# Kernel optimization log

Hardware: AMD Instinct MI355X
Metric: run time of the kernel (lower is better)

Reference implementation:

```python
import jax, jax.numpy as jnp
import numpy as np

DIM = 512
HEADS = 16
WH, WW = 8, 8
B, NW = 8, 64
HD = DIM // HEADS            # 32, head dim
DR = HD // 2                 # 16, rotary dim per spatial axis
LN100 = float(np.log(100.0))


def _axial_freqs():
    # rotary-embedding-torch get_axial_freqs: per-axis freqs (interleaved repeat)
    inv = 1.0 / (10000.0 ** (np.arange(0, DR, 2, dtype=np.float32) / DR))  # (DR/2,)
    fh = np.repeat(np.arange(WH, dtype=np.float32)[:, None] * inv[None, :], 2, axis=-1)  # (WH, DR)
    fw = np.repeat(np.arange(WW, dtype=np.float32)[:, None] * inv[None, :], 2, axis=-1)  # (WW, DR)
    fh = np.broadcast_to(fh[:, None, :], (WH, WW, DR))
    fw = np.broadcast_to(fw[None, :, :], (WH, WW, DR))
    return jnp.asarray(np.concatenate([fh, fw], axis=-1))  # (WH, WW, HD)


def _rotate_half(t):
    # interleaved-pair rotation: (x0,x1) -> (-x1,x0)
    x = t.reshape(t.shape[:-1] + (t.shape[-1] // 2, 2))
    return jnp.stack([-x[..., 1], x[..., 0]], axis=-1).reshape(t.shape)


def _apply_rope(t, freqs):
    return t * jnp.cos(freqs) + _rotate_half(t) * jnp.sin(freqs)


def setup_inputs() -> dict:
    key = jax.random.key(0)
    k0, k1, k2 = jax.random.split(key, 3)
    x = jax.random.normal(k0, (B, NW, WH * WW, DIM), jnp.float32)
    qkv_weight = jax.random.normal(k1, (3 * DIM, DIM), jnp.float32) * 0.02
    q_bias = jnp.zeros((DIM,), jnp.float32)
    v_bias = jnp.zeros((DIM,), jnp.float32)
    logit_scale = jnp.full((HEADS, 1, 1, 1), float(np.log(10.0)), jnp.float32)
    proj_weight = jax.random.normal(k2, (DIM, DIM), jnp.float32) * 0.02
    proj_bias = jnp.zeros((DIM,), jnp.float32)
    return {"x": x, "qkv_weight": qkv_weight, "q_bias": q_bias, "v_bias": v_bias,
            "logit_scale": logit_scale, "proj_weight": proj_weight, "proj_bias": proj_bias}


def reference(x, qkv_weight, q_bias, v_bias, logit_scale, proj_weight, proj_bias):
    Bx, Nw, N, C = x.shape
    qkv_b = jnp.concatenate([q_bias, jnp.zeros_like(v_bias), v_bias])
    qkv = x @ qkv_weight.T + qkv_b                                   # (B, Nw, N, 3C)
    qkv = qkv.reshape(Bx, Nw, N, 3, HEADS, HD).transpose(3, 0, 4, 1, 2, 5)  # (3, B, H, Nw, N, hd)
    q, k, v = qkv[0], qkv[1], qkv[2]
    # cosine attention: L2-normalize q, k
    q = q / jnp.maximum(jnp.linalg.norm(q, axis=-1, keepdims=True), 1e-12)
    k = k / jnp.maximum(jnp.linalg.norm(k, axis=-1, keepdims=True), 1e-12)
    q = jnp.exp(jnp.clip(logit_scale, LN100, None)) * q             # per-head scale, clamp min=ln(100)
    # axial RoPE over the (Wh, Ww) window grid
    freqs = _axial_freqs()                                           # (WH, WW, HD)
    q = _apply_rope(q.reshape(Bx, HEADS, Nw, WH, WW, HD), freqs).reshape(Bx, HEADS, Nw, N, HD)
    k = _apply_rope(k.reshape(Bx, HEADS, Nw, WH, WW, HD), freqs).reshape(Bx, HEADS, Nw, N, HD)
    # block-diagonal (per-window) attention; flex_attention default scale 1/sqrt(hd)
    scores = jnp.einsum('bhwqd,bhwkd->bhwqk', q, k) * (1.0 / np.sqrt(HD))
    attn = jax.nn.softmax(scores, axis=-1)
    out = jnp.einsum('bhwqk,bhwkd->bhwqd', attn, v)                  # (B, H, Nw, N, hd)
    out = out.transpose(0, 2, 3, 1, 4).reshape(Bx, Nw, N, C)
    return out @ proj_weight.T + proj_bias
```

## Files before the change

kernel.cpp:

```cpp
#include <hip/hip_runtime.h>
#include <stdint.h>

#define DIMC   512
#define NHEADS 16
#define HDIM   32
#define NWIN   64
#define NTOK   64
#define NBATCH 8
#define MROWS  (NBATCH * NWIN * NTOK)

typedef unsigned short ushort_t;
typedef __attribute__((ext_vector_type(8))) short short8v;
typedef __attribute__((ext_vector_type(4))) float f32x4;

__device__ inline ushort_t f2bf(float f) {
    unsigned u = __float_as_uint(f);
    u += 0x7FFFu + ((u >> 16) & 1u);
    return (ushort_t)(u >> 16);
}
__device__ inline unsigned packbf2(float a, float b) {
    return ((unsigned)f2bf(a)) | (((unsigned)f2bf(b)) << 16);
}
__device__ inline void unpack8(uint4 u, float* f) {
    const unsigned a[4] = {u.x, u.y, u.z, u.w};
    #pragma unroll
    for (int j = 0; j < 4; ++j) {
        f[2*j+0] = __uint_as_float((a[j] & 0xFFFFu) << 16);
        f[2*j+1] = __uint_as_float(a[j] & 0xFFFF0000u);
    }
}

#define G2L16(gp, lp) __builtin_amdgcn_global_load_lds( \
    (const __attribute__((address_space(1))) unsigned int*)(gp), \
    (__attribute__((address_space(3))) unsigned int*)(lp), 16, 0, 0)

__global__ __launch_bounds__(256) void cvt_f32_bf16(
    const float* __restrict__ in, ushort_t* __restrict__ out, int n4)
{
    int i = blockIdx.x * 256 + threadIdx.x;
    if (i < n4) {
        float4 v = reinterpret_cast<const float4*>(in)[i];
        ushort4 o;
        o.x = f2bf(v.x); o.y = f2bf(v.y); o.z = f2bf(v.z); o.w = f2bf(v.w);
        reinterpret_cast<ushort4*>(out)[i] = o;
    }
}

__global__ void build_qkv_bias(const float* __restrict__ qb,
                               const float* __restrict__ vb,
                               float* __restrict__ bias)
{
    int i = blockIdx.x * 256 + threadIdx.x;
    if (i < 3 * DIMC) {
        float v = 0.f;
        if (i < DIMC) v = qb[i];
        else if (i >= 2 * DIMC) v = vb[i - 2 * DIMC];
        bias[i] = v;
    }
}

template<bool OUT_BF16>
__global__ __launch_bounds__(256) void gemm_bt_128(
    const ushort_t* __restrict__ A, const ushort_t* __restrict__ B,
    const float* __restrict__ bias, void* __restrict__ C,
    int M, int N, int K)
{
    __shared__ ushort_t lsA[128 * 32];
    __shared__ ushort_t lsB[128 * 32];

    const int tid = threadIdx.x;
    const int l   = tid & 63;
    const int wv  = tid >> 6;
    const int wr  = wv >> 1;
    const int wc  = wv & 1;
    const size_t mBase = (size_t)blockIdx.y * 128;
    const size_t nBase = (size_t)blockIdx.x * 128;

    f32x4 acc[4][4] = {};

    const ushort_t* gA0 = A + (mBase + (size_t)(wv * 16 + (l >> 2))) * (size_t)K + (l & 3) * 8;
    const ushort_t* gB0 = B + (nBase + (size_t)(wv * 16 + (l >> 2))) * (size_t)K + (l & 3) * 8;
    ushort_t* lA0 = &lsA[(wv * 16) * 32];
    ushort_t* lB0 = &lsB[(wv * 16) * 32];
    const size_t rowStep = (size_t)64 * (size_t)K;

    for (int k0 = 0; k0 < K; k0 += 32) {
        G2L16(gA0 + k0,           lA0);
        G2L16(gA0 + k0 + rowStep, lA0 + 64 * 32);
        G2L16(gB0 + k0,           lB0);
        G2L16(gB0 + k0 + rowStep, lB0 + 64 * 32);
        __syncthreads();

        short8v aF[4], bF[4];
        #pragma unroll
        for (int m = 0; m < 4; ++m)
            aF[m] = *reinterpret_cast<const short8v*>(
                &lsA[(wr * 64 + m * 16 + (l & 15)) * 32 + (l >> 4) * 8]);
        #pragma unroll
        for (int n = 0; n < 4; ++n)
            bF[n] = *reinterpret_cast<const short8v*>(
                &lsB[(wc * 64 + n * 16 + (l & 15)) * 32 + (l >> 4) * 8]);

        #pragma unroll
        for (int m = 0; m < 4; ++m)
            #pragma unroll
            for (int n = 0; n < 4; ++n)
                acc[m][n] = __builtin_amdgcn_mfma_f32_16x16x32_bf16(
                    aF[m], bF[n], acc[m][n], 0, 0, 0);
        __syncthreads();
    }

    const int c0 = l & 15;
    const int r0 = (l >> 4) * 4;
    #pragma unroll
    for (int m = 0; m < 4; ++m) {
        #pragma unroll
        for (int n = 0; n < 4; ++n) {
            const size_t gn = nBase + (size_t)(wc * 64 + n * 16 + c0);
            const float bv = bias[gn];
            #pragma unroll
            for (int i = 0; i < 4; ++i) {
                const size_t gm = mBase + (size_t)(wr * 64 + m * 16 + r0 + i);
                const float val = acc[m][n][i] + bv;
                if (OUT_BF16) ((ushort_t*)C)[gm * (size_t)N + gn] = f2bf(val);
                else          ((float*)C)  [gm * (size_t)N + gn] = val;
            }
        }
    }
}

__global__ __launch_bounds__(64, 3) void win_attn_mfma(
    const ushort_t* __restrict__ qkv,
    const float* __restrict__ logit_scale,
    ushort_t* __restrict__ attn_out)
{
    __shared__ __align__(16) ushort_t lsP[64 * 64];
    __shared__ __align__(16) ushort_t lsV[2 * 64 * 16];
    __shared__ float2 csT[8][8];

    const int l = threadIdx.x;
    const int c = l & 15;
    const int g = l >> 4;
    const int blk = blockIdx.x;
    const int w = blk & 63;
    const int h = (blk >> 6) & 15;
    const int b = blk >> 10;
    const size_t R = ((size_t)(b * 64 + w)) * 64;
    const ushort_t* qrow = qkv + R * 1536 + h * 32;

    {
        const ushort_t* vbase = qrow + 1024;
        #pragma unroll
        for (int half = 0; half < 2; ++half)
            #pragma unroll
            for (int kg = 0; kg < 2; ++kg) {
                const ushort_t* gsrc = vbase + (size_t)(kg * 32 + (l >> 1)) * 1536
                                       + half * 16 + (l & 1) * 8;
                G2L16(gsrc, &lsV[half * 1024 + kg * 512]);
            }
    }

    {
        const int pos = l >> 3, f = l & 7;
        const float inv = __expf(-(float)f * 1.1512925464970230f);
        const float ang = (float)pos * inv;
        csT[pos][f] = make_float2(__cosf(ang), __sinf(ang));
    }

    const float sc = __expf(fmaxf(logit_scale[h], 4.6051701859880914f))
                     * 0.17677669529663687f;

    short8v Qf[4], Kf[4];
    #pragma unroll
    for (int mi = 0; mi < 4; ++mi) {
        const int tok = mi * 16 + c;
        const ushort_t* qp = qrow + (size_t)tok * 1536 + g * 8;
        uint4 uq = *reinterpret_cast<const uint4*>(qp);
        uint4 uk = *reinterpret_cast<const uint4*>(qp + 512);
        float qv[8], kv[8];
        unpack8(uq, qv); unpack8(uk, kv);

        float sq = 0.f, sk = 0.f;
        #pragma unroll
        for (int d = 0; d < 8; ++d) { sq += qv[d] * qv[d]; sk += kv[d] * kv[d]; }
        sq += __shfl_xor(sq, 16); sq += __shfl_xor(sq, 32);
        sk += __shfl_xor(sk, 16); sk += __shfl_xor(sk, 32);
        const float qs = sc * rsqrtf(fmaxf(sq, 1e-24f));
        const float ks =      rsqrtf(fmaxf(sk, 1e-24f));

        const int wh = tok >> 3, ww = tok & 7;
        const int axpos = (g >= 2) ? ww : wh;
        union { short8v v; unsigned u[4]; } pq, pk2;
        #pragma unroll
        for (int pp = 0; pp < 4; ++pp) {
            const float2 cs = csT[axpos][(g & 1) * 4 + pp];
            float a0 = qv[2*pp] * qs, a1 = qv[2*pp+1] * qs;
            const float q0 = a0 * cs.x - a1 * cs.y;
            const float q1 = a1 * cs.x + a0 * cs.y;
            a0 = kv[2*pp] * ks; a1 = kv[2*pp+1] * ks;
            const float k0 = a0 * cs.x - a1 * cs.y;
            const float k1 = a1 * cs.x + a0 * cs.y;
            pq.u[pp]  = packbf2(q0, q1);
            pk2.u[pp] = packbf2(k0, k1);
        }
        Qf[mi] = pq.v; Kf[mi] = pk2.v;
    }

    f32x4 S[4][4];
    #pragma unroll
    for (int ki = 0; ki < 4; ++ki)
        #pragma unroll
        for (int qi = 0; qi < 4; ++qi)
            S[ki][qi] = __builtin_amdgcn_mfma_f32_16x16x32_bf16(
                Kf[ki], Qf[qi], (f32x4){0.f, 0.f, 0.f, 0.f}, 0, 0, 0);

    float isum[4];
    #pragma unroll
    for (int qi = 0; qi < 4; ++qi) {
        float m = -1e30f;
        #pragma unroll
        for (int ki = 0; ki < 4; ++ki)
            #pragma unroll
            for (int i = 0; i < 4; ++i) m = fmaxf(m, S[ki][qi][i]);
        m = fmaxf(m, __shfl_xor(m, 16));
        m = fmaxf(m, __shfl_xor(m, 32));
        float sum = 0.f;
        #pragma unroll
        for (int ki = 0; ki < 4; ++ki)
            #pragma unroll
            for (int i = 0; i < 4; ++i) {
                const float p = __expf(S[ki][qi][i] - m);
                S[ki][qi][i] = p; sum += p;
            }
        sum += __shfl_xor(sum, 16); sum += __shfl_xor(sum, 32);
        isum[qi] = 1.0f / sum;
    }

    #pragma unroll
    for (int qi = 0; qi < 4; ++qi) {
        const int q = qi * 16 + c;
        #pragma unroll
        for (int ki = 0; ki < 4; ++ki) {
            const int s2 = 2 * ki + (g >> 1);
            const int byteoff = q * 128 + ((s2 ^ (q & 7)) * 16) + (g & 1) * 8;
            uint2 pk2;
            pk2.x = packbf2(S[ki][qi][0], S[ki][qi][1]);
            pk2.y = packbf2(S[ki][qi][2], S[ki][qi][3]);
            *reinterpret_cast<uint2*>(reinterpret_cast<char*>(lsP) + byteoff) = pk2;
        }
    }

    asm volatile("s_waitcnt vmcnt(0)" ::: "memory");
    short8v Vf[2][2];
    #pragma unroll
    for (int half = 0; half < 2; ++half)
        #pragma unroll
        for (int ki = 0; ki < 2; ++ki) {
            union { short8v v; ushort_t e[8]; } t;
            #pragma unroll
            for (int j = 0; j < 8; ++j)
                t.e[j] = lsV[half * 1024 + (ki * 32 + g * 8 + j) * 16 + c];
            Vf[half][ki] = t.v;
        }

    short8v Pf[4][2];
    #pragma unroll
    for (int ni = 0; ni < 4; ++ni) {
        const int q = ni * 16 + c;
        #pragma unroll
        for (int ki = 0; ki < 2; ++ki) {
            const int s2 = ki * 4 + g;
            Pf[ni][ki] = *reinterpret_cast<const short8v*>(
                reinterpret_cast<const char*>(lsP) + q * 128 + ((s2 ^ (q & 7)) * 16));
        }
    }

    f32x4 O[2][4];
    #pragma unroll
    for (int mi = 0; mi < 2; ++mi)
        #pragma unroll
        for (int ni = 0; ni < 4; ++ni) {
            f32x4 a = __builtin_amdgcn_mfma_f32_16x16x32_bf16(
                Vf[mi][0], Pf[ni][0], (f32x4){0.f, 0.f, 0.f, 0.f}, 0, 0, 0);
            O[mi][ni] = __builtin_amdgcn_mfma_f32_16x16x32_bf16(
                Vf[mi][1], Pf[ni][1], a, 0, 0, 0);
        }

    #pragma unroll
    for (int ni = 0; ni < 4; ++ni) {
        const int q = ni * 16 + c;
        const float is = isum[ni];
        #pragma unroll
        for (int mi = 0; mi < 2; ++mi) {
            const int s = 2 * mi + (g >> 1);
            const int byteoff = q * 64 + ((s ^ (q & 3)) * 16) + (g & 1) * 8;
            uint2 pk2;
            pk2.x = packbf2(O[mi][ni][0] * is, O[mi][ni][1] * is);
            pk2.y = packbf2(O[mi][ni][2] * is, O[mi][ni][3] * is);
            *reinterpret_cast<uint2*>(reinterpret_cast<char*>(lsP) + byteoff) = pk2;
        }
    }

    const int qr0 = l >> 2, p = l & 3;
    ushort_t* obase = attn_out + R * 512 + h * 32;
    #pragma unroll
    for (int r = 0; r < 4; ++r) {
        const int q = qr0 + r * 16;
        uint4 row = *reinterpret_cast<const uint4*>(
            reinterpret_cast<const char*>(lsP) + q * 64 + ((p ^ (q & 3)) * 16));
        *reinterpret_cast<uint4*>(
            reinterpret_cast<char*>(obase + (size_t)q * 512) + p * 16) = row;
    }
}

extern "C" void kernel_launch(void* const* d_in, const int* in_sizes, int n_in,
                              void* d_out, int out_size, void* d_ws, size_t ws_size,
                              hipStream_t stream)
{
    (void)in_sizes; (void)n_in; (void)out_size; (void)ws_size;
    const float* x     = (const float*)d_in[0];
    const float* wqkv  = (const float*)d_in[1];
    const float* qb    = (const float*)d_in[2];
    const float* vb    = (const float*)d_in[3];
    const float* ls    = (const float*)d_in[4];
    const float* wproj = (const float*)d_in[5];
    const float* pb    = (const float*)d_in[6];
    float* out = (float*)d_out;

    char* ws = (char*)d_ws;
    ushort_t* xb      = (ushort_t*)(ws);
    ushort_t* wqkvb   = (ushort_t*)(ws + 33554432);
    ushort_t* wprojb  = (ushort_t*)(ws + 35127296);
    ushort_t* qkvb    = (ushort_t*)(ws + 35651584);
    ushort_t* attnb   = (ushort_t*)(ws + 136314880);
    float*    qkvbias = (float*)   (ws + 169869312);

    cvt_f32_bf16<<<16384, 256, 0, stream>>>(x,     xb,     16777216 / 4);
    cvt_f32_bf16<<<768,   256, 0, stream>>>(wqkv,  wqkvb,  786432   / 4);
    cvt_f32_bf16<<<256,   256, 0, stream>>>(wproj, wprojb, 262144   / 4);
    build_qkv_bias<<<6, 256, 0, stream>>>(qb, vb, qkvbias);

    gemm_bt_128<true><<<dim3(12, 256), 256, 0, stream>>>(
        xb, wqkvb, qkvbias, qkvb, MROWS, 3 * DIMC, DIMC);

    win_attn_mfma<<<NBATCH * NHEADS * NWIN, 64, 0, stream>>>(qkvb, ls, attnb);

    gemm_bt_128<false><<<dim3(4, 256), 256, 0, stream>>>(
        attnb, wprojb, pb, out, MROWS, DIMC, DIMC);
}
```

Measured before the change: 276.7 us.

## Double GEMM K-tile to 64 with XOR-swizzled LDS layout

The bf16 GEMM kernels now stage a 64-wide K slice per iteration instead of 32, halving the number of barrier pairs per output tile and issuing twice as many MFMAs between syncs. The LDS layout is XOR-swizzled by row so that 16-byte fragment reads from the 128-byte rows avoid bank conflicts. Shared memory per block doubles to 32 KB, which may reduce how many blocks fit per CU.

New measurement: 271.2 us. 2.0% less time.

```diff
diff --git a/kernel.cpp b/kernel.cpp
--- a/kernel.cpp
+++ b/kernel.cpp
@@ -60,13 +60,13 @@
 }
 
 template<bool OUT_BF16>
-__global__ __launch_bounds__(256) void gemm_bt_128(
+__global__ __launch_bounds__(256) void gemm_bt_128x64(
     const ushort_t* __restrict__ A, const ushort_t* __restrict__ B,
     const float* __restrict__ bias, void* __restrict__ C,
     int M, int N, int K)
 {
-    __shared__ ushort_t lsA[128 * 32];
-    __shared__ ushort_t lsB[128 * 32];
+    __shared__ ushort_t lsA[128 * 64];
+    __shared__ ushort_t lsB[128 * 64];
 
     const int tid = threadIdx.x;
     const int l   = tid & 63;
@@ -78,35 +78,45 @@
 
     f32x4 acc[4][4] = {};
 
-    const ushort_t* gA0 = A + (mBase + (size_t)(wv * 16 + (l >> 2))) * (size_t)K + (l & 3) * 8;
-    const ushort_t* gB0 = B + (nBase + (size_t)(wv * 16 + (l >> 2))) * (size_t)K + (l & 3) * 8;
-    ushort_t* lA0 = &lsA[(wv * 16) * 32];
-    ushort_t* lB0 = &lsB[(wv * 16) * 32];
-    const size_t rowStep = (size_t)64 * (size_t)K;
-
-    for (int k0 = 0; k0 < K; k0 += 32) {
-        G2L16(gA0 + k0,           lA0);
-        G2L16(gA0 + k0 + rowStep, lA0 + 64 * 32);
-        G2L16(gB0 + k0,           lB0);
-        G2L16(gB0 + k0 + rowStep, lB0 + 64 * 32);
+    const int rl    = l >> 3;
+    const int chunk = (l & 7) ^ rl;
+    const ushort_t* gA0 = A + (mBase + (size_t)(wv * 32 + rl)) * (size_t)K + chunk * 8;
+    const ushort_t* gB0 = B + (nBase + (size_t)(wv * 32 + rl)) * (size_t)K + chunk * 8;
+    ushort_t* lA0 = &lsA[(wv * 32) * 64];
+    ushort_t* lB0 = &lsB[(wv * 32) * 64];
+
+    for (int k0 = 0; k0 < K; k0 += 64) {
+        #pragma unroll
+        for (int j = 0; j < 4; ++j) {
+            G2L16(gA0 + (size_t)(j * 8) * (size_t)K + k0, lA0 + j * 8 * 64);
+            G2L16(gB0 + (size_t)(j * 8) * (size_t)K + k0, lB0 + j * 8 * 64);
+        }
         __syncthreads();
 
-        short8v aF[4], bF[4];
-        #pragma unroll
-        for (int m = 0; m < 4; ++m)
-            aF[m] = *reinterpret_cast<const short8v*>(
-                &lsA[(wr * 64 + m * 16 + (l & 15)) * 32 + (l >> 4) * 8]);
-        #pragma unroll
-        for (int n = 0; n < 4; ++n)
-            bF[n] = *reinterpret_cast<const short8v*>(
-                &lsB[(wc * 64 + n * 16 + (l & 15)) * 32 + (l >> 4) * 8]);
-
-        #pragma unroll
-        for (int m = 0; m < 4; ++m)
-            #pragma unroll
-            for (int n = 0; n < 4; ++n)
-                acc[m][n] = __builtin_amdgcn_mfma_f32_16x16x32_bf16(
-                    aF[m], bF[n], acc[m][n], 0, 0, 0);
+        #pragma unroll
+        for (int kk = 0; kk < 2; ++kk) {
+            short8v aF[4], bF[4];
+            #pragma unroll
+            for (int m = 0; m < 4; ++m) {
+                const int row = wr * 64 + m * 16 + (l & 15);
+                const int ps  = (kk * 4 + (l >> 4)) ^ (row & 7);
+                aF[m] = *reinterpret_cast<const short8v*>(
+                    reinterpret_cast<const char*>(lsA) + row * 128 + ps * 16);
+            }
+            #pragma unroll
+            for (int n = 0; n < 4; ++n) {
+                const int row = wc * 64 + n * 16 + (l & 15);
+                const int ps  = (kk * 4 + (l >> 4)) ^ (row & 7);
+                bF[n] = *reinterpret_cast<const short8v*>(
+                    reinterpret_cast<const char*>(lsB) + row * 128 + ps * 16);
+            }
+            #pragma unroll
+            for (int m = 0; m < 4; ++m)
+                #pragma unroll
+                for (int n = 0; n < 4; ++n)
+                    acc[m][n] = __builtin_amdgcn_mfma_f32_16x16x32_bf16(
+                        aF[m], bF[n], acc[m][n], 0, 0, 0);
+        }
         __syncthreads();
     }
 
@@ -340,11 +350,11 @@
     cvt_f32_bf16<<<256,   256, 0, stream>>>(wproj, wprojb, 262144   / 4);
     build_qkv_bias<<<6, 256, 0, stream>>>(qb, vb, qkvbias);
 
-    gemm_bt_128<true><<<dim3(12, 256), 256, 0, stream>>>(
+    gemm_bt_128x64<true><<<dim3(12, 256), 256, 0, stream>>>(
         xb, wqkvb, qkvbias, qkvb, MROWS, 3 * DIMC, DIMC);
 
     win_attn_mfma<<<NBATCH * NHEADS * NWIN, 64, 0, stream>>>(qkvb, ls, attnb);
 
-    gemm_bt_128<false><<<dim3(4, 256), 256, 0, stream>>>(
+    gemm_bt_128x64<false><<<dim3(4, 256), 256, 0, stream>>>(
         attnb, wprojb, pb, out, MROWS, DIMC, DIMC);
 }
```

## Replace GEMM with 256x256 double-buffered, swizzled, phase-pipelined MFMA kernel

Applied to the files above, without the earlier changes.

Both projection GEMMs move from a 128x128 single-buffered tile kernel to a 512-thread 256x256 tile kernel with BK=64. It double-buffers LDS, uses XOR-swizzled LDS layouts, and splits each K step into four phases that interleave global-to-LDS staging with MFMA quadrants under explicit barriers and waitcnts. The block index is remapped across XCD-style groups, and MFMA sections raise wave priority. This aims to hide memory latency and increase reuse, at the cost of large LDS use (128KB per block), lower occupancy and fragile manual synchronisation. A __syncthreads is also added in the attention kernel before LDS reuse.

Measured after the change: 285.2 us. 1.03x slower.

```diff
diff --git a/kernel.cpp b/kernel.cpp
--- a/kernel.cpp
+++ b/kernel.cpp
@@ -59,68 +59,133 @@
     }
 }
 
+#define BARX() { asm volatile("" ::: "memory"); \
+                 __builtin_amdgcn_s_barrier();  \
+                 asm volatile("" ::: "memory"); }
+#define LGKM0() asm volatile("s_waitcnt lgkmcnt(0)" ::: "memory")
+#define VMW(n)  asm volatile("s_waitcnt vmcnt(" #n ")" ::: "memory")
+
+#define STAGE(ls, g, bufi, t, h)                                             \
+    {                                                                        \
+        const int _k0 = (t) << 6;                                            \
+        _Pragma("unroll")                                                    \
+        for (int _r = 0; _r < 2; ++_r)                                       \
+            G2L16(g + (size_t)((h) * 128 + _r * 64) * (size_t)K + _k0,       \
+                  &ls[bufi][((h) * 128 + _r * 64 + wv * 8) * 64]);           \
+    }
+
+#define DSA(dst, bufi, mh)                                                   \
+    _Pragma("unroll")                                                        \
+    for (int _m = 0; _m < 4; ++_m) {                                         \
+        _Pragma("unroll")                                                    \
+        for (int _k = 0; _k < 2; ++_k) {                                     \
+            const int _row = wr * 128 + ((mh) * 4 + _m) * 16 + (l & 15);     \
+            const int _ps  = (_k * 4 + (l >> 4)) ^ (_row & 7);               \
+            dst[_m * 2 + _k] = *reinterpret_cast<const short8v*>(            \
+                reinterpret_cast<const char*>(lsA[bufi]) + _row * 128 + _ps * 16); \
+        }                                                                    \
+    }
+
+#define DSB(dst, bufi, nh)                                                   \
+    _Pragma("unroll")                                                        \
+    for (int _n = 0; _n < 2; ++_n) {                                         \
+        _Pragma("unroll")                                                    \
+        for (int _k = 0; _k < 2; ++_k) {                                     \
+            const int _row = wc * 64 + ((nh) * 2 + _n) * 16 + (l & 15);      \
+            const int _ps  = (_k * 4 + (l >> 4)) ^ (_row & 7);               \
+            dst[_n * 2 + _k] = *reinterpret_cast<const short8v*>(            \
+                reinterpret_cast<const char*>(lsB[bufi]) + _row * 128 + _ps * 16); \
+        }                                                                    \
+    }
+
+#define MMQ(af, bf, mo, no)                                                  \
+    __builtin_amdgcn_s_setprio(1);                                           \
+    _Pragma("unroll")                                                        \
+    for (int _m = 0; _m < 4; ++_m) {                                         \
+        _Pragma("unroll")                                                    \
+        for (int _n = 0; _n < 2; ++_n) {                                     \
+            _Pragma("unroll")                                                \
+            for (int _k = 0; _k < 2; ++_k)                                   \
+                acc[(mo) + _m][(no) + _n] =                                  \
+                    __builtin_amdgcn_mfma_f32_16x16x32_bf16(                 \
+                        af[_m * 2 + _k], bf[_n * 2 + _k],                    \
+                        acc[(mo) + _m][(no) + _n], 0, 0, 0);                 \
+        }                                                                    \
+    }                                                                        \
+    __builtin_amdgcn_s_setprio(0);
+
 template<bool OUT_BF16>
-__global__ __launch_bounds__(256) void gemm_bt_128(
+__global__ __launch_bounds__(512, 2) void gemm_bt_8ph(
     const ushort_t* __restrict__ A, const ushort_t* __restrict__ B,
     const float* __restrict__ bias, void* __restrict__ C,
-    int M, int N, int K)
+    int N, int K, int nx)
 {
-    __shared__ ushort_t lsA[128 * 32];
-    __shared__ ushort_t lsB[128 * 32];
+    __shared__ ushort_t lsA[2][256 * 64];
+    __shared__ ushort_t lsB[2][256 * 64];
 
     const int tid = threadIdx.x;
     const int l   = tid & 63;
     const int wv  = tid >> 6;
-    const int wr  = wv >> 1;
-    const int wc  = wv & 1;
-    const size_t mBase = (size_t)blockIdx.y * 128;
-    const size_t nBase = (size_t)blockIdx.x * 128;
-
-    f32x4 acc[4][4] = {};
-
-    const ushort_t* gA0 = A + (mBase + (size_t)(wv * 16 + (l >> 2))) * (size_t)K + (l & 3) * 8;
-    const ushort_t* gB0 = B + (nBase + (size_t)(wv * 16 + (l >> 2))) * (size_t)K + (l & 3) * 8;
-    ushort_t* lA0 = &lsA[(wv * 16) * 32];
-    ushort_t* lB0 = &lsB[(wv * 16) * 32];
-    const size_t rowStep = (size_t)64 * (size_t)K;
-
-    for (int k0 = 0; k0 < K; k0 += 32) {
-        G2L16(gA0 + k0,           lA0);
-        G2L16(gA0 + k0 + rowStep, lA0 + 64 * 32);
-        G2L16(gB0 + k0,           lB0);
-        G2L16(gB0 + k0 + rowStep, lB0 + 64 * 32);
-        __syncthreads();
-
-        short8v aF[4], bF[4];
-        #pragma unroll
-        for (int m = 0; m < 4; ++m)
-            aF[m] = *reinterpret_cast<const short8v*>(
-                &lsA[(wr * 64 + m * 16 + (l & 15)) * 32 + (l >> 4) * 8]);
-        #pragma unroll
-        for (int n = 0; n < 4; ++n)
-            bF[n] = *reinterpret_cast<const short8v*>(
-                &lsB[(wc * 64 + n * 16 + (l & 15)) * 32 + (l >> 4) * 8]);
-
-        #pragma unroll
-        for (int m = 0; m < 4; ++m)
-            #pragma unroll
-            for (int n = 0; n < 4; ++n)
-                acc[m][n] = __builtin_amdgcn_mfma_f32_16x16x32_bf16(
-                    aF[m], bF[n], acc[m][n], 0, 0, 0);
-        __syncthreads();
+    const int wr  = wv >> 2;
+    const int wc  = wv & 3;
+
+    const int nwg = (int)gridDim.x;
+    const int bid = (int)blockIdx.x;
+    const int swz = (bid & 7) * (nwg >> 3) + (bid >> 3);
+    const size_t mBase = (size_t)(swz / nx) * 256;
+    const size_t nBase = (size_t)(swz % nx) * 256;
+
+    f32x4 acc[8][4] = {};
+
+    const int srow   = l >> 3;
+    const int schunk = (l & 7) ^ srow;
+    const ushort_t* gA = A + (mBase + (size_t)(wv * 8 + srow)) * (size_t)K + schunk * 8;
+    const ushort_t* gB = B + (nBase + (size_t)(wv * 8 + srow)) * (size_t)K + schunk * 8;
+
+    STAGE(lsA, gA, 0, 0, 0); STAGE(lsA, gA, 0, 0, 1);
+    STAGE(lsB, gB, 0, 0, 0); STAGE(lsB, gB, 0, 0, 1);
+    STAGE(lsB, gB, 1, 1, 0); STAGE(lsB, gB, 1, 1, 1);
+    VMW(4);
+    BARX();
+
+    short8v aF[8], bF[4], bF2[4];
+    const int nt = K >> 6;
+    for (int t = 0; t < nt; ++t) {
+        const int buf = t & 1, nbuf = buf ^ 1;
+        DSA(aF, buf, 0);
+        DSB(bF, buf, 0);
+        if (t + 1 < nt) STAGE(lsA, gA, nbuf, t + 1, 0);
+        BARX(); LGKM0();
+        MMQ(aF, bF, 0, 0);
+        BARX();
+        DSB(bF2, buf, 1);
+        if (t + 1 < nt) STAGE(lsA, gA, nbuf, t + 1, 1);
+        BARX(); LGKM0();
+        MMQ(aF, bF2, 0, 2);
+        BARX();
+        DSA(aF, buf, 1);
+        if (t + 2 < nt) STAGE(lsB, gB, buf, t + 2, 0);
+        BARX(); LGKM0();
+        MMQ(aF, bF, 4, 0);
+        BARX();
+        if (t + 2 < nt) { STAGE(lsB, gB, buf, t + 2, 1); VMW(4); }
+        else if (t + 1 < nt) { VMW(0); }
+        BARX();
+        MMQ(aF, bF2, 4, 2);
+        BARX();
     }
 
     const int c0 = l & 15;
     const int r0 = (l >> 4) * 4;
     #pragma unroll
-    for (int m = 0; m < 4; ++m) {
-        #pragma unroll
-        for (int n = 0; n < 4; ++n) {
-            const size_t gn = nBase + (size_t)(wc * 64 + n * 16 + c0);
-            const float bv = bias[gn];
+    for (int n = 0; n < 4; ++n) {
+        const size_t gn = nBase + (size_t)(wc * 64 + n * 16 + c0);
+        const float bv = bias[gn];
+        #pragma unroll
+        for (int m = 0; m < 8; ++m) {
             #pragma unroll
             for (int i = 0; i < 4; ++i) {
-                const size_t gm = mBase + (size_t)(wr * 64 + m * 16 + r0 + i);
+                const size_t gm = mBase + (size_t)(wr * 128 + m * 16 + r0 + i);
                 const float val = acc[m][n][i] + bv;
                 if (OUT_BF16) ((ushort_t*)C)[gm * (size_t)N + gn] = f2bf(val);
                 else          ((float*)C)  [gm * (size_t)N + gn] = val;
@@ -286,6 +351,7 @@
                 Vf[mi][1], Pf[ni][1], a, 0, 0, 0);
         }
 
+    __syncthreads();
     #pragma unroll
     for (int ni = 0; ni < 4; ++ni) {
         const int q = ni * 16 + c;
@@ -340,11 +406,11 @@
     cvt_f32_bf16<<<256,   256, 0, stream>>>(wproj, wprojb, 262144   / 4);
     build_qkv_bias<<<6, 256, 0, stream>>>(qb, vb, qkvbias);
 
-    gemm_bt_128<true><<<dim3(12, 256), 256, 0, stream>>>(
-        xb, wqkvb, qkvbias, qkvb, MROWS, 3 * DIMC, DIMC);
+    gemm_bt_8ph<true><<<768, 512, 0, stream>>>(
+        xb, wqkvb, qkvbias, qkvb, 3 * DIMC, DIMC, 6);
 
     win_attn_mfma<<<NBATCH * NHEADS * NWIN, 64, 0, stream>>>(qkvb, ls, attnb);
 
-    gemm_bt_128<false><<<dim3(4, 256), 256, 0, stream>>>(
-        attnb, wprojb, pb, out, MROWS, DIMC, DIMC);
-}
+    gemm_bt_8ph<false><<<256, 512, 0, stream>>>(
+        attnb, wprojb, pb, out, DIMC, DIMC, 2);
+}
```
